# Performance work log

Measured on AMD Instinct MI355X. Metric: run time of the kernel, lower is better.

## Reference

```python
import jax, jax.numpy as jnp
import numpy as np

B, G, CE, D, L, H, DH, M, KQ = 4, 64, 384, 512, 8, 16, 32, 2048, 16
NJ, NB = 163, 11
DET_THRESH = 0.3
PATCH = 14.0
EPS = 1e-8


def _ln(x, g, b):
    mu = x.mean(-1, keepdims=True)
    v = x.var(-1, keepdims=True)
    return (x - mu) * jax.lax.rsqrt(v + 1e-5) * g + b


def setup_inputs():
    key = jax.random.key(0)
    ks = iter(jax.random.split(key, 64))
    def n(sh, s=0.02):
        return (jax.random.normal(next(ks), sh) * s).astype(jnp.float32)
    inp = {}
    inp['feat'] = jax.random.normal(next(ks), (B, G, G, CE), dtype=jnp.float32)
    inp['scores'] = jax.random.uniform(next(ks), (B, G, G), dtype=jnp.float32)
    inp['K_cam'] = jnp.tile(jnp.array([[1000., 0., 448.], [0., 1000., 448.], [0., 0., 1.]], dtype=jnp.float32), (B, 1, 1))
    inp['pos_emb'] = n((G * G, D), 1.0)
    inp['Wtok'] = n((CE, D)); inp['btok'] = jnp.zeros((D,), jnp.float32)
    for nm in ['Wq', 'Wk', 'Wv', 'Wo']:
        inp[nm] = n((L, D, D))
    inp['g1'] = jnp.ones((L, D), jnp.float32); inp['b1n'] = jnp.zeros((L, D), jnp.float32)
    inp['W1'] = n((L, D, M)); inp['bf1'] = jnp.zeros((L, M), jnp.float32)
    inp['W2'] = n((L, M, D)); inp['bf2'] = jnp.zeros((L, D), jnp.float32)
    inp['g2'] = jnp.ones((L, D), jnp.float32); inp['b2n'] = jnp.zeros((L, D), jnp.float32)
    inp['offW1'] = n((D, D)); inp['offb1'] = jnp.zeros((D,), jnp.float32)
    inp['offW2'] = n((D, 2)); inp['offb2'] = jnp.zeros((2,), jnp.float32)
    inp['dW1'] = n((D, D)); inp['db1'] = jnp.zeros((D,), jnp.float32)
    inp['dW2'] = n((D, 1)); inp['db2'] = jnp.zeros((1,), jnp.float32)
    inp['sW1'] = n((D, D)); inp['sb1'] = jnp.zeros((D,), jnp.float32)
    inp['sW2'] = n((D, NB)); inp['sb2'] = jnp.zeros((NB,), jnp.float32)
    inp['pW1'] = n((D + NJ * 6, D)); inp['pb1'] = jnp.zeros((D,), jnp.float32)
    inp['pW2'] = n((D, NJ * 6)); inp['pb2'] = jnp.zeros((NJ * 6,), jnp.float32)
    # identity-like 6D init pose per joint: eye(3)[:, :2].flatten() = [1,0,0,1,0,0]
    inp['init_body_pose'] = jnp.tile(jnp.array([1., 0., 0., 1., 0., 0.], dtype=jnp.float32), NJ)
    inp['useful_rotmat'] = (jax.random.uniform(next(ks), (NJ,)) < 0.66).astype(jnp.float32)
    return inp


def reference(feat, scores, K_cam, pos_emb, Wtok, btok,
              Wq, Wk, Wv, Wo, g1, b1n, W1, bf1, W2, bf2, g2, b2n,
              offW1, offb1, offW2, offb2, dW1, db1, dW2, db2,
              sW1, sb1, sW2, sb2, pW1, pb1, pW2, pb2,
              init_body_pose, useful_rotmat):
    # --- NMS via 3x3 max-pool (stride 1, same padding) + threshold ---
    sm = jax.lax.reduce_window(scores, -jnp.inf, jax.lax.max, (1, 3, 3), (1, 1, 1), 'SAME')
    sc = scores * (sm == scores).astype(scores.dtype)
    flat = sc.reshape(B, G * G)
    vals, idx = jax.lax.top_k(flat, KQ)                 # padded ragged detections
    mask = (vals >= DET_THRESH).astype(feat.dtype)      # [B,KQ] validity mask
    row = idx // G
    col = idx % G
    # --- token projection + 2d pos emb, gather queries ---
    dec_emb = feat @ Wtok + btok + pos_emb.reshape(G, G, D)        # [B,G,G,D]
    ctx = dec_emb.reshape(B, G * G, D)                              # context per image
    q = jnp.take_along_axis(ctx, idx[..., None], axis=1)            # [B,KQ,D]
    x = q * mask[..., None]
    scale = DH ** -0.5
    # --- HPH decoder: depth x (prenorm cross-attn to full-image context + FFN) ---
    for l in range(L):
        h = _ln(x, g1[l], b1n[l])
        qh = (h @ Wq[l]).reshape(B, KQ, H, DH)
        kh = (ctx @ Wk[l]).reshape(B, G * G, H, DH)
        vh = (ctx @ Wv[l]).reshape(B, G * G, H, DH)
        att = jax.nn.softmax(jnp.einsum('bqhd,bkhd->bhqk', qh, kh) * scale, axis=-1)
        o = jnp.einsum('bhqk,bkhd->bqhd', att, vh).reshape(B, KQ, H * DH) @ Wo[l]
        x = x + o * mask[..., None]
        h2 = _ln(x, g2[l], b2n[l])
        x = x + (jax.nn.gelu(h2 @ W1[l] + bf1[l]) @ W2[l] + bf2[l]) * mask[..., None]
    y = x.reshape(B * KQ, D)
    m = mask.reshape(B * KQ, 1)
    # --- heads ---
    offset = jax.nn.relu(y @ offW1 + offb1) @ offW2 + offb2          # [N,2]
    loc_coarse = jnp.stack([col.reshape(-1), row.reshape(-1)], -1).astype(y.dtype)
    loc = (loc_coarse + 0.5 + offset) * PATCH
    Kd = jnp.repeat(K_cam, KQ, axis=0)                               # [N,3,3]
    focal = Kd[:, 0, 0]
    d_raw = jax.nn.relu(y @ dW1 + db1) @ dW2 + db2                   # [N,1]
    dist = focal[:, None] / jnp.clip(jnp.exp(d_raw), 1e-5)
    homo = jnp.concatenate([loc, jnp.ones_like(loc[:, :1])], -1)     # [N,3]
    Kinv = jnp.linalg.inv(Kd)
    transl = jnp.einsum('nij,nj->ni', Kinv, homo) * dist             # [N,3]
    shape_ = jax.nn.sigmoid(jax.nn.relu(y @ sW1 + sb1) @ sW2 + sb2)  # [N,11]
    ibp = jnp.broadcast_to(init_body_pose, (B * KQ, NJ * 6))
    rot6d = jax.nn.relu(jnp.concatenate([y, ibp], -1) @ pW1 + pb1) @ pW2 + pb2 + ibp
    # --- special Gram-Schmidt: 6D -> rotation matrices ---
    Mm = rot6d.reshape(-1, NJ, 3, 2)
    u0 = Mm[..., 0]
    u0 = u0 / (jnp.linalg.norm(u0, axis=-1, keepdims=True) + EPS)
    v1 = Mm[..., 1] - jnp.sum(Mm[..., 1] * u0, -1, keepdims=True) * u0
    u1 = v1 / (jnp.linalg.norm(v1, axis=-1, keepdims=True) + EPS)
    u2 = jnp.cross(u0, u1)
    rotmat = jnp.stack([u0, u1, u2], -1)                             # [N,NJ,3,3]
    eye = jnp.eye(3, dtype=rotmat.dtype)
    um = useful_rotmat.reshape(1, NJ, 1, 1)
    rotmat = um * rotmat + (1.0 - um) * eye
    out = jnp.concatenate([loc, offset, dist, transl, shape_, rotmat.reshape(B * KQ, NJ * 9)], -1) * m
    return out
```

## Files before the change

### kernel.cpp

```cpp
#include <hip/hip_runtime.h>

typedef unsigned int uint;
typedef unsigned short u16;

#define BB 4
#define CE 384
#define DD 512
#define LL 8
#define HH 16
#define MM 2048
#define NJ 163
#define TOK 4096
#define BKQ 64
#define QH 256
#define OUTW 1486
#define NROT 978
#define QKSCALE 0.17677669529663687f

typedef __attribute__((ext_vector_type(8))) short short8;
typedef __attribute__((ext_vector_type(4))) float float4v;

static __device__ __forceinline__ u16 f2bf(float f){
  union { float f; uint u; } c; c.f = f;
  uint u = c.u;
// ... 6 lines not shown
static __device__ __forceinline__ float wred_sum(float v){
  for (int o = 32; o; o >>= 1) v += __shfl_xor(v, o, 64);
  return v;
}
static __device__ __forceinline__ void gl16(const void* g, void* l){
  __builtin_amdgcn_global_load_lds((const __attribute__((address_space(1))) void*)g,
                                   (__attribute__((address_space(3))) void*)l, 16, 0, 0);
}

__global__ __launch_bounds__(256) void k_nms_topk(const float* __restrict__ scores,
    int* __restrict__ oidx, float* __restrict__ omask, float* __restrict__ ocol, float* __restrict__ orow)
{
  int b = blockIdx.x, t = threadIdx.x;
  __shared__ float sraw[4096];
  __shared__ float sv[4]; __shared__ int si[4]; __shared__ int swin;
  const float* sp = scores + (size_t)b * 4096;
  for (int i = t; i < 4096; i += 256) sraw[i] = sp[i];
  __syncthreads();
  float v[16];
  #pragma unroll
  for (int j = 0; j < 16; j++){
    int i = t + j*256;
    int r = i >> 6, c = i & 63;
    float mx = -1e30f;
    for (int dr = -1; dr <= 1; dr++){
      int rr = r + dr; if (rr < 0 || rr > 63) continue;
      for (int dc = -1; dc <= 1; dc++){
        int cc = c + dc; if (cc < 0 || cc > 63) continue;
        mx = fmaxf(mx, sraw[rr*64+cc]);
      }
    }
    float s = sraw[i];
    v[j] = (s == mx) ? s : 0.0f;
  }
  int lane = t & 63, wv = t >> 6;
  for (int iter = 0; iter < 16; iter++){
    float best = -1e30f; int bi_ = 1 << 30;
    #pragma unroll
    for (int j = 0; j < 16; j++){
      if (v[j] > best){ best = v[j]; bi_ = t + j*256; }
    }
    #pragma unroll
    for (int o = 32; o; o >>= 1){
      float ov = __shfl_xor(best, o, 64);
      int oi = __shfl_xor(bi_, o, 64);
      if (ov > best || (ov == best && oi < bi_)){ best = ov; bi_ = oi; }
    }
    if (lane == 0){ sv[wv] = best; si[wv] = bi_; }
    __syncthreads();
    if (t == 0){
      float bb = sv[0]; int ii = si[0];
      for (int k = 1; k < 4; k++){
        if (sv[k] > bb || (sv[k] == bb && si[k] < ii)){ bb = sv[k]; ii = si[k]; }
      }
      oidx[b*16+iter] = ii;
      omask[b*16+iter] = (bb >= 0.3f) ? 1.f : 0.f;
      ocol[b*16+iter] = (float)(ii & 63);
      orow[b*16+iter] = (float)(ii >> 6);
      swin = ii;
    }
    __syncthreads();
    int wi = swin;
    if ((wi & 255) == t) v[wi >> 8] = -1e30f;
    __syncthreads();
  }
}

__global__ __launch_bounds__(256) void k_cvt_bf16(const float* __restrict__ in, u16* __restrict__ out, int n4){
  int i = blockIdx.x*256 + threadIdx.x;
  int stride = gridDim.x*256;
  for (int j = i; j < n4; j += stride){
    float4 v = ((const float4*)in)[j];
    ushort4 o;
    o.x = f2bf(v.x); o.y = f2bf(v.y); o.z = f2bf(v.z); o.w = f2bf(v.w);
    ((ushort4*)out)[j] = o;
  }
}

struct PJobs {
  const float* s[24]; u16* d[24];
  int R[24], C[24], t0[25];
  int njobs, ntiles;
};
__global__ __launch_bounds__(256) void k_prepw(PJobs J){
  __shared__ float tile[32][33];
  for (int g = blockIdx.x; g < J.ntiles; g += gridDim.x){
    int j = 0;
    while (g >= J.t0[j+1]) j++;
    int ti = g - J.t0[j];
    int C_ = J.C[j], R_ = J.R[j];
    int tC = (C_ + 31) >> 5;
    int ry = ti / tC, cx = ti - ry*tC;
    int c0 = cx*32, r0 = ry*32;
    int tx = threadIdx.x & 31, ty = threadIdx.x >> 5;
    const float* src = J.s[j]; u16* dst = J.d[j];
    for (int i = 0; i < 32; i += 8){
      float v = 0.f;
      if (c0+tx < C_) v = src[(size_t)(r0+ty+i)*C_ + c0+tx];
      tile[ty+i][tx] = v;
    }
    __syncthreads();
    for (int i = 0; i < 32; i += 8){
      if (c0+ty+i < C_) dst[(size_t)(c0+ty+i)*R_ + r0+tx] = f2bf(tile[tx][ty+i]);
    }
    __syncthreads();
  }
}

__global__ __launch_bounds__(256) void k_transp_b(const u16* __restrict__ in, u16* __restrict__ out, int R, int C){
  in  += (size_t)blockIdx.z * R * C;
  out += (size_t)blockIdx.z * R * C;
  __shared__ u16 tile[32][33];
  int c0 = blockIdx.x*32, r0 = blockIdx.y*32;
  int tx = threadIdx.x & 31, ty = threadIdx.x >> 5;
  for (int i = 0; i < 32; i += 8) tile[ty+i][tx] = in[(size_t)(r0+ty+i)*C + c0+tx];
  __syncthreads();
  for (int i = 0; i < 32; i += 8) out[(size_t)(c0+ty+i)*R + r0+tx] = tile[tx][ty+i];
}

__global__ __launch_bounds__(256) void k_wqk(const float* __restrict__ wq, const float* __restrict__ wk,
    u16* __restrict__ AT)
{
  __shared__ __align__(16) u16 As[2560];
  __shared__ __align__(16) u16 Bs[2560];
  int id = blockIdx.x, t = threadIdx.x;
  int rt = id & 127, dt = id >> 7;
  int h = rt >> 3, dout0 = (rt & 7)*64, din0 = dt*64;
  int r = t >> 2, c0 = (t & 3)*8;
  {
    float4 u0 = *(const float4*)(wk + (size_t)(dout0+r)*DD + h*32 + c0);
    float4 u1 = *(const float4*)(wk + (size_t)(dout0+r)*DD + h*32 + c0 + 4);
    u16* d = As + r*40 + c0;
    d[0]=f2bf(u0.x); d[1]=f2bf(u0.y); d[2]=f2bf(u0.z); d[3]=f2bf(u0.w);
    d[4]=f2bf(u1.x); d[5]=f2bf(u1.y); d[6]=f2bf(u1.z); d[7]=f2bf(u1.w);
    float4 v0 = *(const float4*)(wq + (size_t)(din0+r)*DD + h*32 + c0);
    float4 v1 = *(const float4*)(wq + (size_t)(din0+r)*DD + h*32 + c0 + 4);
    u16* e = Bs + r*40 + c0;
    e[0]=f2bf(v0.x); e[1]=f2bf(v0.y); e[2]=f2bf(v0.z); e[3]=f2bf(v0.w);
    e[4]=f2bf(v1.x); e[5]=f2bf(v1.y); e[6]=f2bf(v1.z); e[7]=f2bf(v1.w);
  }
  __syncthreads();
  int lane = t & 63, w = t >> 6, lr = lane & 15, lk = lane >> 4;
  short8 af = *(const short8*)&As[(w*16+lr)*40 + lk*8];
  float4v acc[4];
  float4v z4 = {0.f,0.f,0.f,0.f};
  acc[0]=z4; acc[1]=z4; acc[2]=z4; acc[3]=z4;
  #pragma unroll
  for (int nf = 0; nf < 4; nf++){
    short8 bf8 = *(const short8*)&Bs[(nf*16+lr)*40 + lk*8];
    acc[nf] = __builtin_amdgcn_mfma_f32_16x16x32_bf16(af, bf8, acc[nf], 0, 0, 0);
  }
  #pragma unroll
  for (int nf = 0; nf < 4; nf++){
    #pragma unroll
    for (int jj = 0; jj < 4; jj++){
      int row = w*16 + lk*4 + jj;
      AT[(size_t)(h*512 + dout0 + row)*DD + din0 + nf*16 + lr] = f2bf(acc[nf][jj]*QKSCALE);
    }
  }
}

__global__ __launch_bounds__(256) void k_wvo(const float* __restrict__ wv, const float* __restrict__ wo,
    u16* __restrict__ WVOT)
{
  __shared__ __align__(16) u16 As[2560];
  __shared__ __align__(16) u16 Bs[2560];
  int id = blockIdx.x, t = threadIdx.x;
  int ct = id & 127, dt = id >> 7;
  int h = ct >> 3, Dc0 = (ct & 7)*64, dout0 = dt*64;
  {
    int c = t >> 3, d8 = (t & 7)*8;
    float4 a0 = *(const float4*)(wo + (size_t)(h*32+c)*DD + dout0 + d8);
    float4 a1 = *(const float4*)(wo + (size_t)(h*32+c)*DD + dout0 + d8 + 4);
    As[(d8+0)*40 + c] = f2bf(a0.x);
    As[(d8+1)*40 + c] = f2bf(a0.y);
    As[(d8+2)*40 + c] = f2bf(a0.z);
    As[(d8+3)*40 + c] = f2bf(a0.w);
    As[(d8+4)*40 + c] = f2bf(a1.x);
    As[(d8+5)*40 + c] = f2bf(a1.y);
    As[(d8+6)*40 + c] = f2bf(a1.z);
    As[(d8+7)*40 + c] = f2bf(a1.w);
    int r = t >> 2, c0 = (t & 3)*8;
    float4 v0 = *(const float4*)(wv + (size_t)(Dc0+r)*DD + h*32 + c0);
    float4 v1 = *(const float4*)(wv + (size_t)(Dc0+r)*DD + h*32 + c0 + 4);
    u16* e = Bs + r*40 + c0;
    e[0]=f2bf(v0.x); e[1]=f2bf(v0.y); e[2]=f2bf(v0.z); e[3]=f2bf(v0.w);
    e[4]=f2bf(v1.x); e[5]=f2bf(v1.y); e[6]=f2bf(v1.z); e[7]=f2bf(v1.w);
  }
  __syncthreads();
  int lane = t & 63, w = t >> 6, lr = lane & 15, lk = lane >> 4;
  short8 af = *(const short8*)&As[(w*16+lr)*40 + lk*8];
  float4v acc[4];
  float4v z4 = {0.f,0.f,0.f,0.f};
  acc[0]=z4; acc[1]=z4; acc[2]=z4; acc[3]=z4;
  #pragma unroll
  for (int nf = 0; nf < 4; nf++){
    short8 bf8 = *(const short8*)&Bs[(nf*16+lr)*40 + lk*8];
    acc[nf] = __builtin_amdgcn_mfma_f32_16x16x32_bf16(af, bf8, acc[nf], 0, 0, 0);
  }
  #pragma unroll
  for (int nf = 0; nf < 4; nf++){
    #pragma unroll
    for (int jj = 0; jj < 4; jj++){
      int row = w*16 + lk*4 + jj;
      WVOT[(size_t)(dout0 + row)*8192 + h*512 + Dc0 + nf*16 + lr] = f2bf(acc[nf][jj]);
    }
  }
}

__global__ __launch_bounds__(256) void k_red8(const float* __restrict__ parts, u16* __restrict__ cf){
  int i4 = blockIdx.x*256 + threadIdx.x;
  int elem = i4*4;
  int row = elem >> 13, col = elem & 8191;
  int b = row >> 4, q = row & 15, h = col >> 9, Dc = col & 511;
  const float* src = parts + ((size_t)b*8)*131072 + (size_t)(q*16+h)*512 + Dc;
  float4 s = *(const float4*)src;
  #pragma unroll
  for (int ks = 1; ks < 8; ks++){
    float4 g = *(const float4*)(src + (size_t)ks*131072);
    s.x += g.x; s.y += g.y; s.z += g.z; s.w += g.w;
  }
  ushort4 o;
  o.x = f2bf(s.x); o.y = f2bf(s.y); o.z = f2bf(s.z); o.w = f2bf(s.w);
  *(ushort4*)&cf[(size_t)row*8192 + col] = o;
}

__global__ __launch_bounds__(256) void k_gemm_emb(
    const u16* __restrict__ A, const u16* __restrict__ Bt, u16* __restrict__ Cb,
    const float* __restrict__ ep1, const float* __restrict__ ep2)
{
  int m0 = blockIdx.y*128, n0 = blockIdx.x*128;
  __shared__ __align__(16) u16 As[128*64];
  __shared__ __align__(16) u16 Bs[128*64];
  int t = threadIdx.x, lane = t & 63, wave = t >> 6;
  int wr = wave >> 1, wc = wave & 1;
  int lr = lane & 15, lk = lane >> 4;
  int sr8 = t >> 3, sl = t & 7;
  int sw = ((sl ^ (sr8 & 7)) * 8);
  float4v acc[4][4];
  float4v z4 = {0.f, 0.f, 0.f, 0.f};
  #pragma unroll
  for (int i = 0; i < 4; i++)
    #pragma unroll
    for (int j = 0; j < 4; j++) acc[i][j] = z4;
  for (int kt = 0; kt < CE; kt += 64){
    __syncthreads();
    #pragma unroll
    for (int rg = 0; rg < 4; rg++){
      gl16(A + (size_t)(m0 + rg*32 + sr8)*CE + kt + sw, As + rg*2048 + 8*t);
      gl16(Bt + (size_t)(n0 + rg*32 + sr8)*CE + kt + sw, Bs + rg*2048 + 8*t);
    }
    __syncthreads();
    #pragma unroll
    for (int s = 0; s < 2; s++){
      int slot = ((s*4 + lk) ^ (lr & 7)) * 8;
      short8 af[4], bfr[4];
      #pragma unroll
      for (int i = 0; i < 4; i++) af[i] = *(const short8*)&As[(wr*64 + i*16 + lr)*64 + slot];
      #pragma unroll
      for (int j = 0; j < 4; j++) bfr[j] = *(const short8*)&Bs[(wc*64 + j*16 + lr)*64 + slot];
      #pragma unroll
      for (int i = 0; i < 4; i++)
        #pragma unroll
        for (int j = 0; j < 4; j++)
          acc[i][j] = __builtin_amdgcn_mfma_f32_16x16x32_bf16(af[i], bfr[j], acc[i][j], 0, 0, 0);
    }
  }
  #pragma unroll
  for (int i = 0; i < 4; i++){
    int rbase = m0 + wr*64 + i*16 + lk*4;
    #pragma unroll
    for (int j = 0; j < 4; j++){
      int cc = n0 + wc*64 + j*16 + lr;
      #pragma unroll
      for (int jj = 0; jj < 4; jj++){
        int rr = rbase + jj;
        float vv = acc[i][j][jj] + ep1[cc] + ep2[(size_t)(rr & 4095)*DD + cc];
        Cb[(size_t)rr*DD + cc] = f2bf(vv);
      }
    }
  }
}

__global__ __launch_bounds__(256) void k_misc(const float* __restrict__ feat, const float* __restrict__ Wtok,
    const float* __restrict__ btok, const float* __restrict__ pos_emb, const int* __restrict__ oidx,
    float* __restrict__ x, const float* __restrict__ pW1, const float* __restrict__ pb1,
    const float* __restrict__ ibp, float* __restrict__ hb4,
    const float* __restrict__ offb1, const float* __restrict__ db1, const float* __restrict__ sb1,
    const float* __restrict__ pb2, float* __restrict__ cvec2)
{
  int bid = blockIdx.x, t = threadIdx.x;
  if (bid < 64){
    int b = bid >> 4, tok = oidx[bid];
    __shared__ float fs[CE];
    const float* fr = feat + ((size_t)b*TOK + tok) * CE;
    for (int i = t; i < CE; i += 256) fs[i] = fr[i];
    __syncthreads();
    for (int d = t; d < DD; d += 256){
      float acc = btok[d] + pos_emb[(size_t)tok*DD + d];
      for (int i = 0; i < CE; i++) acc += fs[i] * Wtok[(size_t)i*DD + d];
      x[(size_t)bid*DD + d] = acc;
    }
  } else if (bid < 192){
    int d = (bid - 64)*4 + (t >> 6);
    int ln = t & 63;
    float acc = 0.f;
    for (int i = ln; i < NJ*6; i += 64) acc += ibp[i] * pW1[(size_t)(DD+i)*DD + d];
    acc = wred_sum(acc);
    if (ln == 0) hb4[1536 + d] = acc + pb1[d];
  } else {
    for (int i = t; i < 1536; i += 256)
      hb4[i] = (i < 512) ? offb1[i] : (i < 1024 ? db1[i-512] : sb1[i-1024]);
    for (int i = t; i < 1024; i += 256)
      cvec2[i] = (i < NJ*6) ? (pb2[i] + ibp[i]) : 0.f;
  }
}

template<int EPI>
__global__ __launch_bounds__(256) void k_gemm_bt64(
    const u16* __restrict__ A, const u16* __restrict__ Bt,
    float* __restrict__ C, u16* __restrict__ Cb,
    int Kslice, int lda, int ldb, int ldc,
    long sA, long sB, long sC, int ksplit)
{
  int bz = blockIdx.z;
  int batch = bz / ksplit, ks = bz - batch*ksplit;
  const u16* Ab = A + (size_t)batch*sA + (size_t)ks*Kslice;
  const u16* Bb = Bt + (size_t)batch*sB + (size_t)ks*Kslice;
  int m0 = blockIdx.y*128, n0 = blockIdx.x*64;
  __shared__ __align__(16) u16 As[128*64];
  __shared__ __align__(16) u16 Bs[64*64];
  int t = threadIdx.x, lane = t & 63, w = t >> 6;
  int lr = lane & 15, lk = lane >> 4;
  int sr8 = t >> 3, sl = t & 7;
  int sw = ((sl ^ (sr8 & 7)) * 8);
  float4v acc[2][4];
  float4v z4 = {0.f,0.f,0.f,0.f};
  #pragma unroll
  for (int i = 0; i < 2; i++)
    #pragma unroll
    for (int j = 0; j < 4; j++) acc[i][j] = z4;

  for (int kt = 0; kt < Kslice; kt += 64){
    __syncthreads();
    #pragma unroll
    for (int rg = 0; rg < 4; rg++)
      gl16(Ab + (size_t)(m0 + rg*32 + sr8)*lda + kt + sw, As + rg*2048 + 8*t);
    #pragma unroll
    for (int rg = 0; rg < 2; rg++)
      gl16(Bb + (size_t)(n0 + rg*32 + sr8)*ldb + kt + sw, Bs + rg*2048 + 8*t);
    __syncthreads();
    #pragma unroll
    for (int s = 0; s < 2; s++){
      int slot = ((s*4 + lk) ^ (lr & 7)) * 8;
      short8 af[2], bfr[4];
      #pragma unroll
      for (int i = 0; i < 2; i++) af[i] = *(const short8*)&As[(w*32 + i*16 + lr)*64 + slot];
      #pragma unroll
      for (int j = 0; j < 4; j++) bfr[j] = *(const short8*)&Bs[(j*16 + lr)*64 + slot];
      #pragma unroll
      for (int i = 0; i < 2; i++)
        #pragma unroll
        for (int j = 0; j < 4; j++)
          acc[i][j] = __builtin_amdgcn_mfma_f32_16x16x32_bf16(af[i], bfr[j], acc[i][j], 0, 0, 0);
    }
  }
  #pragma unroll
  for (int i = 0; i < 2; i++){
    int rbase = m0 + w*32 + i*16 + lk*4;
    #pragma unroll
    for (int j = 0; j < 4; j++){
      int cc = n0 + j*16 + lr;
      #pragma unroll
      for (int jj = 0; jj < 4; jj++){
        int rr = rbase + jj;
        if (EPI == 0) C[(size_t)bz*sC + (size_t)rr*ldc + cc] = acc[i][j][jj];
        else Cb[(size_t)batch*sC + (size_t)rr*ldc + cc] = f2bf(acc[i][j][jj]);
      }
    }
  }
}

template<int ACT, int RES, int OUTB, int DOLN, int NG, int HPB, int ZMAP = 0>
__global__ __launch_bounds__(256) void k_mf64(
    const u16* __restrict__ A, const float* __restrict__ xf,
    const float* __restrict__ g, const float* __restrict__ bb,
    const u16* __restrict__ Bt, const float* __restrict__ bias,
    float* __restrict__ C, u16* __restrict__ Cb, u16* __restrict__ Cb2,
    int N, int K, int kper, int ldc, float alpha)
{
  __shared__ __align__(16) u16 Asl[DOLN ? 64*520 : 64*64];
  __shared__ __align__(16) u16 Bs[64*64];
  int t = threadIdx.x, lane = t & 63, w = t >> 6;
  int lr = lane & 15, lk = lane >> 4;
  int n0 = blockIdx.x*64;
  int ks = blockIdx.y, kbeg = ks*kper;
  int sr8 = t >> 3, sl = t & 7;
  int sw = ((sl ^ (sr8 & 7)) * 8);

  if (DOLN){
    for (int rr = 0; rr < 16; rr++){
      int row = w*16 + rr;
      const float* xr = xf + (size_t)row*DD;
      float4 v0 = *(const float4*)(xr + lane*4);
      float4 v1 = *(const float4*)(xr + 256 + lane*4);
      float s = v0.x+v0.y+v0.z+v0.w + v1.x+v1.y+v1.z+v1.w;
      s = wred_sum(s);
      float mu = s * (1.f/DD);
      float d0=v0.x-mu, d1=v0.y-mu, d2=v0.z-mu, d3=v0.w-mu;
      float e0=v1.x-mu, e1=v1.y-mu, e2=v1.z-mu, e3=v1.w-mu;
      float q = d0*d0+d1*d1+d2*d2+d3*d3 + e0*e0+e1*e1+e2*e2+e3*e3;
      q = wred_sum(q);
      float inv = rsqrtf(q * (1.f/DD) + 1e-5f);
      float4 g0 = *(const float4*)(g + lane*4);
      float4 g1 = *(const float4*)(g + 256 + lane*4);
      float4 b0 = *(const float4*)(bb + lane*4);
      float4 b1 = *(const float4*)(bb + 256 + lane*4);
      u16* dst = &Asl[row*520];
      dst[lane*4+0] = f2bf(d0*inv*g0.x + b0.x);
      dst[lane*4+1] = f2bf(d1*inv*g0.y + b0.y);
      dst[lane*4+2] = f2bf(d2*inv*g0.z + b0.z);
      dst[lane*4+3] = f2bf(d3*inv*g0.w + b0.w);
      dst[256+lane*4+0] = f2bf(e0*inv*g1.x + b1.x);
      dst[256+lane*4+1] = f2bf(e1*inv*g1.y + b1.y);
      dst[256+lane*4+2] = f2bf(e2*inv*g1.z + b1.z);
      dst[256+lane*4+3] = f2bf(e3*inv*g1.w + b1.w);
    }
  }

  float4v acc[4];
  float4v z4 = {0.f,0.f,0.f,0.f};
  acc[0]=z4; acc[1]=z4; acc[2]=z4; acc[3]=z4;

  for (int kc = kbeg; kc < kbeg + kper; kc += 64){
    __syncthreads();
    if (!DOLN){
      gl16(A + (size_t)sr8*K + kc + sw,        (u16*)Asl + 8*t);
      gl16(A + (size_t)(32+sr8)*K + kc + sw,   (u16*)Asl + 2048 + 8*t);
    }
    gl16(Bt + (size_t)(n0+sr8)*K + kc + sw,      (u16*)Bs + 8*t);
    gl16(Bt + (size_t)(n0+32+sr8)*K + kc + sw,   (u16*)Bs + 2048 + 8*t);
    __syncthreads();
    #pragma unroll
    for (int s = 0; s < 2; s++){
      int slot = ((s*4 + lk) ^ (lr & 7)) * 8;
      short8 af;
      if (DOLN) af = *(const short8*)&Asl[(w*16+lr)*520 + kc + s*32 + lk*8];
      else      af = *(const short8*)&Asl[(w*16+lr)*64 + slot];
      #pragma unroll
      for (int nf = 0; nf < 4; nf++){
        short8 bf8 = *(const short8*)&Bs[(nf*16+lr)*64 + slot];
        acc[nf] = __builtin_amdgcn_mfma_f32_16x16x32_bf16(af, bf8, acc[nf], 0, 0, 0);
      }
    }
  }
  #pragma unroll
  for (int nf = 0; nf < 4; nf++){
    int col = n0 + nf*16 + lr;
    float bsv = (bias && ks == 0) ? bias[col] : 0.f;
    #pragma unroll
// ... 105 lines not shown
    o[0] = l0*m; o[1] = l1*m; o[2] = off0*m; o[3] = off1*m; o[4] = dist*m;
    o[5] = tx*m; o[6] = ty*m; o[7] = dist*m;
    #pragma unroll
    for (int j = 0; j < 11; j++){ float sp = sout[3+j] + sb2[j]; o[8+j] = m / (1.f + expf(-sp)); }
  }
  if (t < NJ){
    const float* rp = rot6d + (size_t)bq*NROT + t*6;
    float a0 = rp[0], b0 = rp[1], a1 = rp[2], b1 = rp[3], a2 = rp[4], b2 = rp[5];
    float n0 = sqrtf(a0*a0 + a1*a1 + a2*a2);
    float i0 = 1.f / (n0 + 1e-8f);
    float u00 = a0*i0, u01 = a1*i0, u02 = a2*i0;
    float dt = b0*u00 + b1*u01 + b2*u02;
    float v0 = b0 - dt*u00, v1 = b1 - dt*u01, v2 = b2 - dt*u02;
    float n1 = sqrtf(v0*v0 + v1*v1 + v2*v2);
    float i1 = 1.f / (n1 + 1e-8f);
    float u10 = v0*i1, u11 = v1*i1, u12 = v2*i1;
    float u20 = u01*u12 - u02*u11;
    float u21 = u02*u10 - u00*u12;
    float u22 = u00*u11 - u01*u10;
    float um = useful[t], om = 1.f - um;
    float R00 = um*u00 + om, R01 = um*u10,      R02 = um*u20;
    float R10 = um*u01,      R11 = um*u11 + om, R12 = um*u21;
    float R20 = um*u02,      R21 = um*u12,      R22 = um*u22 + om;
    float* o = out + (size_t)bq*OUTW + 19 + t*9;
    o[0] = R00*m; o[1] = R01*m; o[2] = R02*m;
    o[3] = R10*m; o[4] = R11*m; o[5] = R12*m;
    o[6] = R20*m; o[7] = R21*m; o[8] = R22*m;
  }
}

extern "C" void kernel_launch(void* const* d_in, const int* in_sizes, int n_in,
                              void* d_out, int out_size, void* d_ws, size_t ws_size,
                              hipStream_t stream)
{
  const float* feat   = (const float*)d_in[0];
  const float* scores = (const float*)d_in[1];
  const float* K_cam  = (const float*)d_in[2];
  const float* pos_emb= (const float*)d_in[3];
  const float* Wtok   = (const float*)d_in[4];
  const float* btok   = (const float*)d_in[5];
  const float* Wq     = (const float*)d_in[6];
  const float* Wk     = (const float*)d_in[7];
  const float* Wv     = (const float*)d_in[8];
  const float* Wo     = (const float*)d_in[9];
  const float* g1     = (const float*)d_in[10];
  const float* b1n    = (const float*)d_in[11];
  const float* W1     = (const float*)d_in[12];
  const float* bf1    = (const float*)d_in[13];
  const float* W2     = (const float*)d_in[14];
  const float* bf2    = (const float*)d_in[15];
  const float* g2     = (const float*)d_in[16];
  const float* b2n    = (const float*)d_in[17];
  const float* offW1  = (const float*)d_in[18];
  const float* offb1  = (const float*)d_in[19];
  const float* offW2  = (const float*)d_in[20];
  const float* offb2  = (const float*)d_in[21];
  const float* dW1    = (const float*)d_in[22];
  const float* db1    = (const float*)d_in[23];
  const float* dW2    = (const float*)d_in[24];
  const float* db2    = (const float*)d_in[25];
  const float* sW1    = (const float*)d_in[26];
  const float* sb1    = (const float*)d_in[27];
  const float* sW2    = (const float*)d_in[28];
  const float* sb2    = (const float*)d_in[29];
  const float* pW1    = (const float*)d_in[30];
  const float* pb1    = (const float*)d_in[31];
  const float* pW2    = (const float*)d_in[32];
  const float* pb2    = (const float*)d_in[33];
  const float* ibp    = (const float*)d_in[34];
  const float* useful = (const float*)d_in[35];
  float* out = (float*)d_out;

  char* wsp = (char*)d_ws;
  size_t off = 0;
  auto alloc = [&](size_t bytes)->char*{
    char* p = wsp + off;
    off += (bytes + 255) & ~((size_t)255);
    return p;
  };
  int*   t_idx  = (int*)  alloc(BKQ*4);
  float* t_mask = (float*)alloc(BKQ*4);
  float* t_col  = (float*)alloc(BKQ*4);
  float* t_row  = (float*)alloc(BKQ*4);
  u16*   feat_bf= (u16*)  alloc((size_t)BB*TOK*CE*2);
  u16*   wtokT  = (u16*)  alloc((size_t)DD*CE*2);
  u16*   ctx_bf = (u16*)  alloc((size_t)BB*TOK*DD*2);
  u16*   ctxT_bf= (u16*)  alloc((size_t)BB*TOK*DD*2);
  u16*   ATb    = (u16*)  alloc((size_t)8192*DD*2);
  u16*   WVOb   = (u16*)  alloc((size_t)DD*8192*2);
  u16*   w1T    = (u16*)  alloc((size_t)LL*DD*MM*2);
  u16*   w2T    = (u16*)  alloc((size_t)LL*MM*DD*2);
  u16*   headsT = (u16*)  alloc((size_t)4*DD*DD*2);
  u16*   pw2T   = (u16*)  alloc((size_t)1024*DD*2);
  float* x      = (float*)alloc((size_t)BKQ*DD*4);
  u16*   x_bf   = (u16*)  alloc((size_t)BKQ*DD*2);
  u16*   z_bf   = (u16*)  alloc((size_t)BKQ*HH*DD*2);
  u16*   logits = (u16*)  alloc((size_t)BB*QH*TOK*2);
  u16*   att_bf = (u16*)  alloc((size_t)BB*QH*TOK*2);
  float* parts  = (float*)alloc((size_t)BB*8*QH*DD*4);
  u16*   c_flat = (u16*)  alloc((size_t)BKQ*8192*2);
  u16*   mid_bf = (u16*)  alloc((size_t)BKQ*MM*2);
  float* h4     = (float*)alloc((size_t)BKQ*2048*4);
  u16*   hp_bf  = (u16*)  alloc((size_t)BKQ*DD*2);
  float* hb4    = (float*)alloc(2048*4);
  float* cvec2  = (float*)alloc(1024*4);
  float* rot6d  = (float*)alloc((size_t)BKQ*NROT*4);
  if (off > ws_size) return;

  PJobs J;
  int ntl = 0, nj = 0;
  auto addjob = [&](const float* s, u16* d, int R, int C){
    J.s[nj] = s; J.d[nj] = d; J.R[nj] = R; J.C[nj] = C; J.t0[nj] = ntl;
    ntl += ((R+31)/32) * ((C+31)/32);
    nj++;
  };
  addjob(Wtok, wtokT, CE, DD);
  for (int l = 0; l < LL; l++) addjob(W1 + (size_t)l*DD*MM, w1T + (size_t)l*MM*DD, DD, MM);
  for (int l = 0; l < LL; l++) addjob(W2 + (size_t)l*MM*DD, w2T + (size_t)l*DD*MM, MM, DD);
  addjob(offW1, headsT,            DD, DD);
  addjob(dW1,   headsT + DD*DD,    DD, DD);
  addjob(sW1,   headsT + 2*DD*DD,  DD, DD);
  addjob(pW1,   headsT + 3*DD*DD,  DD, DD);
  addjob(pW2,   pw2T, DD, NROT);
  J.t0[nj] = ntl; J.njobs = nj; J.ntiles = ntl;

  k_nms_topk<<<BB, 256, 0, stream>>>(scores, t_idx, t_mask, t_col, t_row);
  k_cvt_bf16<<<3072, 256, 0, stream>>>(feat, feat_bf, BB*TOK*CE/4);
  k_prepw<<<2048, 256, 0, stream>>>(J);
  k_gemm_emb<<<dim3(DD/128, (BB*TOK)/128, 1), 256, 0, stream>>>(feat_bf, wtokT, ctx_bf, btok, pos_emb);
  k_transp_b<<<dim3(DD/32, TOK/32, BB), 256, 0, stream>>>(ctx_bf, ctxT_bf, TOK, DD);
  k_misc<<<193, 256, 0, stream>>>(feat, Wtok, btok, pos_emb, t_idx, x, pW1, pb1, ibp, hb4,
                                  offb1, db1, sb1, pb2, cvec2);

  for (int l = 0; l < LL; l++){
    k_wqk<<<1024, 256, 0, stream>>>(Wq + (size_t)l*DD*DD, Wk + (size_t)l*DD*DD, ATb);
    k_mf64<0,0,0,1,0,0,1><<<dim3(128,1), 256, 0, stream>>>(
        nullptr, x, g1 + l*DD, b1n + l*DD, ATb, nullptr,
        nullptr, z_bf, nullptr, 8192, DD, DD, DD, 1.f);
    k_gemm_bt64<1><<<dim3(TOK/64, 2, BB), 256, 0, stream>>>(
        z_bf, ctx_bf, nullptr, logits,
        DD, DD, DD, TOK, (long)QH*DD, (long)TOK*DD, (long)QH*TOK, 1);
    k_softmax<<<BB*QH, 256, 0, stream>>>(logits, att_bf);
    k_gemm_bt64<0><<<dim3(DD/64, 2, BB*8), 256, 0, stream>>>(
        att_bf, ctxT_bf, parts, nullptr,
        TOK/8, TOK, TOK, DD, (long)QH*TOK, (long)DD*TOK, (long)QH*DD, 8);
    k_wvo<<<1024, 256, 0, stream>>>(Wv + (size_t)l*DD*DD, Wo + (size_t)l*DD*DD, WVOb);
    k_red8<<<512, 256, 0, stream>>>(parts, c_flat);
    k_mf64<0,1,0,0,0,0,0><<<dim3(8,16), 256, 0, stream>>>(
        c_flat, nullptr, nullptr, nullptr, WVOb, nullptr,
        x, nullptr, nullptr, DD, 8192, 512, DD, 1.f);
    k_mf64<2,0,1,1,0,0,0><<<dim3(MM/64,1), 256, 0, stream>>>(
        nullptr, x, g2 + l*DD, b2n + l*DD, w1T + (size_t)l*DD*MM, bf1 + l*MM,
        nullptr, mid_bf, nullptr, MM, DD, DD, MM, 1.f);
    k_mf64<0,1,0,0,0,0,0><<<dim3(8,8), 256, 0, stream>>>(
        mid_bf, nullptr, nullptr, nullptr, w2T + (size_t)l*MM*DD, bf2 + l*DD,
        x, nullptr, nullptr, DD, MM, MM/8, DD, 1.f);
  }

  k_cvt_bf16<<<32, 256, 0, stream>>>(x, x_bf, BKQ*DD/4);
  k_mf64<1,0,0,0,0,1,0><<<dim3(32,1), 256, 0, stream>>>(
      x_bf, nullptr, nullptr, nullptr, headsT, hb4,
      h4, nullptr, hp_bf, 2048, DD, DD, 2048, 1.f);
  k_mf64<0,0,0,0,1,0,0><<<dim3(16,1), 256, 0, stream>>>(
      hp_bf, nullptr, nullptr, nullptr, pw2T, cvec2,
      rot6d, nullptr, nullptr, NROT, DD, DD, NROT, 1.f);
  k_final<<<BKQ, 256, 0, stream>>>(h4, rot6d, offW2, offb2, dW2, db2, sW2, sb2,
                                   K_cam, useful, t_mask, t_col, t_row, out);
}
```

Before: 964.6 us.

## Fuse feat conversion and transpose into embed GEMM, merge weight prep kernels, bf16 split-K parts

Converts fp32 feat to bf16 inside the embedding GEMM load and writes the transposed context from shared memory in its epilogue, removing the separate conversion and transpose kernels. Merges the Wq·Wk and Wv·Wo precompute kernels into one launch and folds bias prep into the weight-prep kernel. Stores split-K attention partials in bf16 to halve their traffic, and gathers query tokens from the bf16 context instead of recomputing them in fp32. This trades some precision (bf16 partial sums and initial queries) for fewer launches and less memory traffic.

```diff
diff --git a/kernel.cpp b/kernel.cpp
--- a/kernel.cpp
+++ b/kernel.cpp
@@ -112,9 +112,28 @@
   int R[24], C[24], t0[25];
   int njobs, ntiles;
 };
-__global__ __launch_bounds__(256) void k_prepw(PJobs J){
+__global__ __launch_bounds__(256) void k_prep_all(PJobs J,
+    const float* __restrict__ pW1, const float* __restrict__ pb1,
+    const float* __restrict__ ibp, float* __restrict__ hb4,
+    const float* __restrict__ offb1, const float* __restrict__ db1, const float* __restrict__ sb1,
+    const float* __restrict__ pb2, float* __restrict__ cvec2)
+{
+  int bid = blockIdx.x, t = threadIdx.x;
+  if (bid < 128){
+    int d = bid*4 + (t >> 6);
+    int ln = t & 63;
+    float acc = 0.f;
+    for (int i = ln; i < NJ*6; i += 64) acc += ibp[i] * pW1[(size_t)(DD+i)*DD + d];
+    acc = wred_sum(acc);
+    if (ln == 0) hb4[1536 + d] = acc + pb1[d];
+  } else if (bid == 128){
+    for (int i = t; i < 1536; i += 256)
+      hb4[i] = (i < 512) ? offb1[i] : (i < 1024 ? db1[i-512] : sb1[i-1024]);
+    for (int i = t; i < 1024; i += 256)
+      cvec2[i] = (i < NJ*6) ? (pb2[i] + ibp[i]) : 0.f;
+  }
   __shared__ float tile[32][33];
-  for (int g = blockIdx.x; g < J.ntiles; g += gridDim.x){
+  for (int g = bid; g < J.ntiles; g += gridDim.x){
     int j = 0;
     while (g >= J.t0[j+1]) j++;
     int ti = g - J.t0[j];
@@ -122,7 +141,7 @@
     int tC = (C_ + 31) >> 5;
     int ry = ti / tC, cx = ti - ry*tC;
     int c0 = cx*32, r0 = ry*32;
-    int tx = threadIdx.x & 31, ty = threadIdx.x >> 5;
+    int tx = t & 31, ty = t >> 5;
     const float* src = J.s[j]; u16* dst = J.d[j];
     for (int i = 0; i < 32; i += 8){
       float v = 0.f;
@@ -137,131 +156,116 @@
   }
 }
 
-__global__ __launch_bounds__(256) void k_transp_b(const u16* __restrict__ in, u16* __restrict__ out, int R, int C){
-  in  += (size_t)blockIdx.z * R * C;
-  out += (size_t)blockIdx.z * R * C;
-  __shared__ u16 tile[32][33];
-  int c0 = blockIdx.x*32, r0 = blockIdx.y*32;
-  int tx = threadIdx.x & 31, ty = threadIdx.x >> 5;
-  for (int i = 0; i < 32; i += 8) tile[ty+i][tx] = in[(size_t)(r0+ty+i)*C + c0+tx];
-  __syncthreads();
-  for (int i = 0; i < 32; i += 8) out[(size_t)(c0+ty+i)*R + r0+tx] = tile[tx][ty+i];
-}
-
-__global__ __launch_bounds__(256) void k_wqk(const float* __restrict__ wq, const float* __restrict__ wk,
-    u16* __restrict__ AT)
+__global__ __launch_bounds__(256) void k_wqkvo(const float* __restrict__ wq, const float* __restrict__ wk,
+    const float* __restrict__ wv, const float* __restrict__ wo,
+    u16* __restrict__ AT, u16* __restrict__ WVOT)
 {
   __shared__ __align__(16) u16 As[2560];
   __shared__ __align__(16) u16 Bs[2560];
-  int id = blockIdx.x, t = threadIdx.x;
-  int rt = id & 127, dt = id >> 7;
-  int h = rt >> 3, dout0 = (rt & 7)*64, din0 = dt*64;
-  int r = t >> 2, c0 = (t & 3)*8;
-  {
-    float4 u0 = *(const float4*)(wk + (size_t)(dout0+r)*DD + h*32 + c0);
-    float4 u1 = *(const float4*)(wk + (size_t)(dout0+r)*DD + h*32 + c0 + 4);
-    u16* d = As + r*40 + c0;
-    d[0]=f2bf(u0.x); d[1]=f2bf(u0.y); d[2]=f2bf(u0.z); d[3]=f2bf(u0.w);
-    d[4]=f2bf(u1.x); d[5]=f2bf(u1.y); d[6]=f2bf(u1.z); d[7]=f2bf(u1.w);
-    float4 v0 = *(const float4*)(wq + (size_t)(din0+r)*DD + h*32 + c0);
-    float4 v1 = *(const float4*)(wq + (size_t)(din0+r)*DD + h*32 + c0 + 4);
-    u16* e = Bs + r*40 + c0;
-    e[0]=f2bf(v0.x); e[1]=f2bf(v0.y); e[2]=f2bf(v0.z); e[3]=f2bf(v0.w);
-    e[4]=f2bf(v1.x); e[5]=f2bf(v1.y); e[6]=f2bf(v1.z); e[7]=f2bf(v1.w);
-  }
-  __syncthreads();
+  int t = threadIdx.x;
   int lane = t & 63, w = t >> 6, lr = lane & 15, lk = lane >> 4;
-  short8 af = *(const short8*)&As[(w*16+lr)*40 + lk*8];
   float4v acc[4];
   float4v z4 = {0.f,0.f,0.f,0.f};
   acc[0]=z4; acc[1]=z4; acc[2]=z4; acc[3]=z4;
-  #pragma unroll
-  for (int nf = 0; nf < 4; nf++){
-    short8 bf8 = *(const short8*)&Bs[(nf*16+lr)*40 + lk*8];
-    acc[nf] = __builtin_amdgcn_mfma_f32_16x16x32_bf16(af, bf8, acc[nf], 0, 0, 0);
-  }
-  #pragma unroll
-  for (int nf = 0; nf < 4; nf++){
-    #pragma unroll
-    for (int jj = 0; jj < 4; jj++){
-      int row = w*16 + lk*4 + jj;
-      AT[(size_t)(h*512 + dout0 + row)*DD + din0 + nf*16 + lr] = f2bf(acc[nf][jj]*QKSCALE);
-    }
-  }
-}
-
-__global__ __launch_bounds__(256) void k_wvo(const float* __restrict__ wv, const float* __restrict__ wo,
-    u16* __restrict__ WVOT)
-{
-  __shared__ __align__(16) u16 As[2560];
-  __shared__ __align__(16) u16 Bs[2560];
-  int id = blockIdx.x, t = threadIdx.x;
-  int ct = id & 127, dt = id >> 7;
-  int h = ct >> 3, Dc0 = (ct & 7)*64, dout0 = dt*64;
-  {
-    int c = t >> 3, d8 = (t & 7)*8;
-    float4 a0 = *(const float4*)(wo + (size_t)(h*32+c)*DD + dout0 + d8);
-    float4 a1 = *(const float4*)(wo + (size_t)(h*32+c)*DD + dout0 + d8 + 4);
-    As[(d8+0)*40 + c] = f2bf(a0.x);
-    As[(d8+1)*40 + c] = f2bf(a0.y);
-    As[(d8+2)*40 + c] = f2bf(a0.z);
-    As[(d8+3)*40 + c] = f2bf(a0.w);
-    As[(d8+4)*40 + c] = f2bf(a1.x);
-    As[(d8+5)*40 + c] = f2bf(a1.y);
-    As[(d8+6)*40 + c] = f2bf(a1.z);
-    As[(d8+7)*40 + c] = f2bf(a1.w);
+  if (blockIdx.x < 1024){
+    int id = blockIdx.x;
+    int rt = id & 127, dt = id >> 7;
+    int h = rt >> 3, dout0 = (rt & 7)*64, din0 = dt*64;
     int r = t >> 2, c0 = (t & 3)*8;
-    float4 v0 = *(const float4*)(wv + (size_t)(Dc0+r)*DD + h*32 + c0);
-    float4 v1 = *(const float4*)(wv + (size_t)(Dc0+r)*DD + h*32 + c0 + 4);
-    u16* e = Bs + r*40 + c0;
-    e[0]=f2bf(v0.x); e[1]=f2bf(v0.y); e[2]=f2bf(v0.z); e[3]=f2bf(v0.w);
-    e[4]=f2bf(v1.x); e[5]=f2bf(v1.y); e[6]=f2bf(v1.z); e[7]=f2bf(v1.w);
-  }
-  __syncthreads();
-  int lane = t & 63, w = t >> 6, lr = lane & 15, lk = lane >> 4;
-  short8 af = *(const short8*)&As[(w*16+lr)*40 + lk*8];
-  float4v acc[4];
-  float4v z4 = {0.f,0.f,0.f,0.f};
-  acc[0]=z4; acc[1]=z4; acc[2]=z4; acc[3]=z4;
-  #pragma unroll
-  for (int nf = 0; nf < 4; nf++){
-    short8 bf8 = *(const short8*)&Bs[(nf*16+lr)*40 + lk*8];
-    acc[nf] = __builtin_amdgcn_mfma_f32_16x16x32_bf16(af, bf8, acc[nf], 0, 0, 0);
-  }
-  #pragma unroll
-  for (int nf = 0; nf < 4; nf++){
-    #pragma unroll
-    for (int jj = 0; jj < 4; jj++){
-      int row = w*16 + lk*4 + jj;
-      WVOT[(size_t)(dout0 + row)*8192 + h*512 + Dc0 + nf*16 + lr] = f2bf(acc[nf][jj]);
-    }
-  }
-}
-
-__global__ __launch_bounds__(256) void k_red8(const float* __restrict__ parts, u16* __restrict__ cf){
+    {
+      float4 u0 = *(const float4*)(wk + (size_t)(dout0+r)*DD + h*32 + c0);
+      float4 u1 = *(const float4*)(wk + (size_t)(dout0+r)*DD + h*32 + c0 + 4);
+      u16* d = As + r*40 + c0;
+      d[0]=f2bf(u0.x); d[1]=f2bf(u0.y); d[2]=f2bf(u0.z); d[3]=f2bf(u0.w);
+      d[4]=f2bf(u1.x); d[5]=f2bf(u1.y); d[6]=f2bf(u1.z); d[7]=f2bf(u1.w);
+      float4 v0 = *(const float4*)(wq + (size_t)(din0+r)*DD + h*32 + c0);
+      float4 v1 = *(const float4*)(wq + (size_t)(din0+r)*DD + h*32 + c0 + 4);
+      u16* e = Bs + r*40 + c0;
+      e[0]=f2bf(v0.x); e[1]=f2bf(v0.y); e[2]=f2bf(v0.z); e[3]=f2bf(v0.w);
+      e[4]=f2bf(v1.x); e[5]=f2bf(v1.y); e[6]=f2bf(v1.z); e[7]=f2bf(v1.w);
+    }
+    __syncthreads();
+    short8 af = *(const short8*)&As[(w*16+lr)*40 + lk*8];
+    #pragma unroll
+    for (int nf = 0; nf < 4; nf++){
+      short8 bf8 = *(const short8*)&Bs[(nf*16+lr)*40 + lk*8];
+      acc[nf] = __builtin_amdgcn_mfma_f32_16x16x32_bf16(af, bf8, acc[nf], 0, 0, 0);
+    }
+    #pragma unroll
+    for (int nf = 0; nf < 4; nf++){
+      #pragma unroll
+      for (int jj = 0; jj < 4; jj++){
+        int row = w*16 + lk*4 + jj;
+        AT[(size_t)(h*512 + dout0 + row)*DD + din0 + nf*16 + lr] = f2bf(acc[nf][jj]*QKSCALE);
+      }
+    }
+  } else {
+    int id = blockIdx.x - 1024;
+    int ct = id & 127, dt = id >> 7;
+    int h = ct >> 3, Dc0 = (ct & 7)*64, dout0 = dt*64;
+    {
+      int c = t >> 3, d8 = (t & 7)*8;
+      float4 a0 = *(const float4*)(wo + (size_t)(h*32+c)*DD + dout0 + d8);
+      float4 a1 = *(const float4*)(wo + (size_t)(h*32+c)*DD + dout0 + d8 + 4);
+      As[(d8+0)*40 + c] = f2bf(a0.x);
+      As[(d8+1)*40 + c] = f2bf(a0.y);
+      As[(d8+2)*40 + c] = f2bf(a0.z);
+      As[(d8+3)*40 + c] = f2bf(a0.w);
+      As[(d8+4)*40 + c] = f2bf(a1.x);
+      As[(d8+5)*40 + c] = f2bf(a1.y);
+      As[(d8+6)*40 + c] = f2bf(a1.z);
+      As[(d8+7)*40 + c] = f2bf(a1.w);
+      int r = t >> 2, c0 = (t & 3)*8;
+      float4 v0 = *(const float4*)(wv + (size_t)(Dc0+r)*DD + h*32 + c0);
+      float4 v1 = *(const float4*)(wv + (size_t)(Dc0+r)*DD + h*32 + c0 + 4);
+      u16* e = Bs + r*40 + c0;
+      e[0]=f2bf(v0.x); e[1]=f2bf(v0.y); e[2]=f2bf(v0.z); e[3]=f2bf(v0.w);
+      e[4]=f2bf(v1.x); e[5]=f2bf(v1.y); e[6]=f2bf(v1.z); e[7]=f2bf(v1.w);
+    }
+    __syncthreads();
+    short8 af = *(const short8*)&As[(w*16+lr)*40 + lk*8];
+    #pragma unroll
+    for (int nf = 0; nf < 4; nf++){
+      short8 bf8 = *(const short8*)&Bs[(nf*16+lr)*40 + lk*8];
+      acc[nf] = __builtin_amdgcn_mfma_f32_16x16x32_bf16(af, bf8, acc[nf], 0, 0, 0);
+    }
+    #pragma unroll
+    for (int nf = 0; nf < 4; nf++){
+      #pragma unroll
+      for (int jj = 0; jj < 4; jj++){
+        int row = w*16 + lk*4 + jj;
+        WVOT[(size_t)(dout0 + row)*8192 + h*512 + Dc0 + nf*16 + lr] = f2bf(acc[nf][jj]);
+      }
+    }
+  }
+}
+
+__global__ __launch_bounds__(256) void k_red8(const u16* __restrict__ parts, u16* __restrict__ cf){
   int i4 = blockIdx.x*256 + threadIdx.x;
   int elem = i4*4;
   int row = elem >> 13, col = elem & 8191;
   int b = row >> 4, q = row & 15, h = col >> 9, Dc = col & 511;
-  const float* src = parts + ((size_t)b*8)*131072 + (size_t)(q*16+h)*512 + Dc;
-  float4 s = *(const float4*)src;
-  #pragma unroll
-  for (int ks = 1; ks < 8; ks++){
-    float4 g = *(const float4*)(src + (size_t)ks*131072);
-    s.x += g.x; s.y += g.y; s.z += g.z; s.w += g.w;
+  const u16* src = parts + ((size_t)b*8)*131072 + (size_t)(q*16+h)*512 + Dc;
+  float s0 = 0.f, s1 = 0.f, s2 = 0.f, s3 = 0.f;
+  #pragma unroll
+  for (int ks = 0; ks < 8; ks++){
+    ushort4 g = *(const ushort4*)(src + (size_t)ks*131072);
+    s0 += bf2f(g.x); s1 += bf2f(g.y); s2 += bf2f(g.z); s3 += bf2f(g.w);
   }
   ushort4 o;
-  o.x = f2bf(s.x); o.y = f2bf(s.y); o.z = f2bf(s.z); o.w = f2bf(s.w);
+  o.x = f2bf(s0); o.y = f2bf(s1); o.z = f2bf(s2); o.w = f2bf(s3);
   *(ushort4*)&cf[(size_t)row*8192 + col] = o;
 }
 
 __global__ __launch_bounds__(256) void k_gemm_emb(
-    const u16* __restrict__ A, const u16* __restrict__ Bt, u16* __restrict__ Cb,
+    const float* __restrict__ feat, const u16* __restrict__ Bt,
+    u16* __restrict__ ctx, u16* __restrict__ ctxT,
     const float* __restrict__ ep1, const float* __restrict__ ep2)
 {
+  __shared__ __align__(16) u16 SM[16640];
+  u16* As = SM;
+  u16* Bs = SM + 8192;
   int m0 = blockIdx.y*128, n0 = blockIdx.x*128;
-  __shared__ __align__(16) u16 As[128*64];
-  __shared__ __align__(16) u16 Bs[128*64];
   int t = threadIdx.x, lane = t & 63, wave = t >> 6;
   int wr = wave >> 1, wc = wave & 1;
   int lr = lane & 15, lk = lane >> 4;
@@ -276,10 +280,16 @@
   for (int kt = 0; kt < CE; kt += 64){
     __syncthreads();
     #pragma unroll
-    for (int rg = 0; rg < 4; rg++){
-      gl16(A + (size_t)(m0 + rg*32 + sr8)*CE + kt + sw, As + rg*2048 + 8*t);
+    for (int p = 0; p < 8; p++){
+      int r = (t >> 4) + p*16, f4 = t & 15;
+      float4 v = *(const float4*)&feat[(size_t)(m0+r)*CE + kt + f4*4];
+      int dc = ((f4 >> 1) ^ (r & 7))*8 + (f4 & 1)*4;
+      ushort4 o; o.x = f2bf(v.x); o.y = f2bf(v.y); o.z = f2bf(v.z); o.w = f2bf(v.w);
+      *(ushort4*)&As[r*64 + dc] = o;
+    }
+    #pragma unroll
+    for (int rg = 0; rg < 4; rg++)
       gl16(Bt + (size_t)(n0 + rg*32 + sr8)*CE + kt + sw, Bs + rg*2048 + 8*t);
-    }
     __syncthreads();
     #pragma unroll
     for (int s = 0; s < 2; s++){
@@ -296,6 +306,7 @@
           acc[i][j] = __builtin_amdgcn_mfma_f32_16x16x32_bf16(af[i], bfr[j], acc[i][j], 0, 0, 0);
     }
   }
+  __syncthreads();
   #pragma unroll
   for (int i = 0; i < 4; i++){
     int rbase = m0 + wr*64 + i*16 + lk*4;
@@ -306,44 +317,31 @@
       for (int jj = 0; jj < 4; jj++){
         int rr = rbase + jj;
         float vv = acc[i][j][jj] + ep1[cc] + ep2[(size_t)(rr & 4095)*DD + cc];
-        Cb[(size_t)rr*DD + cc] = f2bf(vv);
+        u16 bv = f2bf(vv);
+        ctx[(size_t)rr*DD + cc] = bv;
+        SM[(cc - n0)*130 + (rr - m0)] = bv;
       }
     }
   }
-}
-
-__global__ __launch_bounds__(256) void k_misc(const float* __restrict__ feat, const float* __restrict__ Wtok,
-    const float* __restrict__ btok, const float* __restrict__ pos_emb, const int* __restrict__ oidx,
-    float* __restrict__ x, const float* __restrict__ pW1, const float* __restrict__ pb1,
-    const float* __restrict__ ibp, float* __restrict__ hb4,
-    const float* __restrict__ offb1, const float* __restrict__ db1, const float* __restrict__ sb1,
-    const float* __restrict__ pb2, float* __restrict__ cvec2)
-{
-  int bid = blockIdx.x, t = threadIdx.x;
-  if (bid < 64){
-    int b = bid >> 4, tok = oidx[bid];
-    __shared__ float fs[CE];
-    const float* fr = feat + ((size_t)b*TOK + tok) * CE;
-    for (int i = t; i < CE; i += 256) fs[i] = fr[i];
-    __syncthreads();
-    for (int d = t; d < DD; d += 256){
-      float acc = btok[d] + pos_emb[(size_t)tok*DD + d];
-      for (int i = 0; i < CE; i++) acc += fs[i] * Wtok[(size_t)i*DD + d];
-      x[(size_t)bid*DD + d] = acc;
-    }
-  } else if (bid < 192){
-    int d = (bid - 64)*4 + (t >> 6);
-    int ln = t & 63;
-    float acc = 0.f;
-    for (int i = ln; i < NJ*6; i += 64) acc += ibp[i] * pW1[(size_t)(DD+i)*DD + d];
-    acc = wred_sum(acc);
-    if (ln == 0) hb4[1536 + d] = acc + pb1[d];
-  } else {
-    for (int i = t; i < 1536; i += 256)
-      hb4[i] = (i < 512) ? offb1[i] : (i < 1024 ? db1[i-512] : sb1[i-1024]);
-    for (int i = t; i < 1024; i += 256)
-      cvec2[i] = (i < NJ*6) ? (pb2[i] + ibp[i]) : 0.f;
-  }
+  __syncthreads();
+  int b = m0 >> 12, tok0 = m0 & 4095;
+  int tx = t & 63, ty = t >> 6;
+  #pragma unroll 4
+  for (int it = 0; it < 32; it++){
+    int c = ty*32 + it;
+    uint vv = *(const uint*)&SM[c*130 + tx*2];
+    *(uint*)&ctxT[((size_t)b*DD + n0 + c)*TOK + tok0 + tx*2] = vv;
+  }
+}
+
+__global__ __launch_bounds__(256) void k_gather2(const u16* __restrict__ ctx, const int* __restrict__ oidx,
+    float* __restrict__ x)
+{
+  int bq = blockIdx.x, t = threadIdx.x;
+  int b = bq >> 4, tok = oidx[bq];
+  uint v = ((const uint*)(ctx + ((size_t)b*TOK + tok)*DD))[t];
+  float2 o; o.x = bf2f((u16)(v & 0xFFFF)); o.y = bf2f((u16)(v >> 16));
+  *(float2*)&x[(size_t)bq*DD + t*2] = o;
 }
 
 template<int EPI>
@@ -405,7 +403,8 @@
       for (int jj = 0; jj < 4; jj++){
         int rr = rbase + jj;
         if (EPI == 0) C[(size_t)bz*sC + (size_t)rr*ldc + cc] = acc[i][j][jj];
-        else Cb[(size_t)batch*sC + (size_t)rr*ldc + cc] = f2bf(acc[i][j][jj]);
+        else if (EPI == 1) Cb[(size_t)batch*sC + (size_t)rr*ldc + cc] = f2bf(acc[i][j][jj]);
+        else Cb[(size_t)bz*sC + (size_t)rr*ldc + cc] = f2bf(acc[i][j][jj]);
       }
     }
   }
@@ -677,7 +676,6 @@
   float* t_mask = (float*)alloc(BKQ*4);
   float* t_col  = (float*)alloc(BKQ*4);
   float* t_row  = (float*)alloc(BKQ*4);
-  u16*   feat_bf= (u16*)  alloc((size_t)BB*TOK*CE*2);
   u16*   wtokT  = (u16*)  alloc((size_t)DD*CE*2);
   u16*   ctx_bf = (u16*)  alloc((size_t)BB*TOK*DD*2);
   u16*   ctxT_bf= (u16*)  alloc((size_t)BB*TOK*DD*2);
@@ -692,7 +690,7 @@
   u16*   z_bf   = (u16*)  alloc((size_t)BKQ*HH*DD*2);
   u16*   logits = (u16*)  alloc((size_t)BB*QH*TOK*2);
   u16*   att_bf = (u16*)  alloc((size_t)BB*QH*TOK*2);
-  float* parts  = (float*)alloc((size_t)BB*8*QH*DD*4);
+  u16*   parts  = (u16*)  alloc((size_t)BB*8*QH*DD*2);
   u16*   c_flat = (u16*)  alloc((size_t)BKQ*8192*2);
   u16*   mid_bf = (u16*)  alloc((size_t)BKQ*MM*2);
   float* h4     = (float*)alloc((size_t)BKQ*2048*4);
@@ -720,15 +718,13 @@
   J.t0[nj] = ntl; J.njobs = nj; J.ntiles = ntl;
 
   k_nms_topk<<<BB, 256, 0, stream>>>(scores, t_idx, t_mask, t_col, t_row);
-  k_cvt_bf16<<<3072, 256, 0, stream>>>(feat, feat_bf, BB*TOK*CE/4);
-  k_prepw<<<2048, 256, 0, stream>>>(J);
-  k_gemm_emb<<<dim3(DD/128, (BB*TOK)/128, 1), 256, 0, stream>>>(feat_bf, wtokT, ctx_bf, btok, pos_emb);
-  k_transp_b<<<dim3(DD/32, TOK/32, BB), 256, 0, stream>>>(ctx_bf, ctxT_bf, TOK, DD);
-  k_misc<<<193, 256, 0, stream>>>(feat, Wtok, btok, pos_emb, t_idx, x, pW1, pb1, ibp, hb4,
-                                  offb1, db1, sb1, pb2, cvec2);
+  k_prep_all<<<2048, 256, 0, stream>>>(J, pW1, pb1, ibp, hb4, offb1, db1, sb1, pb2, cvec2);
+  k_gemm_emb<<<dim3(DD/128, (BB*TOK)/128, 1), 256, 0, stream>>>(feat, wtokT, ctx_bf, ctxT_bf, btok, pos_emb);
+  k_gather2<<<BKQ, 256, 0, stream>>>(ctx_bf, t_idx, x);
 
   for (int l = 0; l < LL; l++){
-    k_wqk<<<1024, 256, 0, stream>>>(Wq + (size_t)l*DD*DD, Wk + (size_t)l*DD*DD, ATb);
+    k_wqkvo<<<2048, 256, 0, stream>>>(Wq + (size_t)l*DD*DD, Wk + (size_t)l*DD*DD,
+                                      Wv + (size_t)l*DD*DD, Wo + (size_t)l*DD*DD, ATb, WVOb);
     k_mf64<0,0,0,1,0,0,1><<<dim3(128,1), 256, 0, stream>>>(
         nullptr, x, g1 + l*DD, b1n + l*DD, ATb, nullptr,
         nullptr, z_bf, nullptr, 8192, DD, DD, DD, 1.f);
@@ -736,10 +732,9 @@
         z_bf, ctx_bf, nullptr, logits,
         DD, DD, DD, TOK, (long)QH*DD, (long)TOK*DD, (long)QH*TOK, 1);
     k_softmax<<<BB*QH, 256, 0, stream>>>(logits, att_bf);
-    k_gemm_bt64<0><<<dim3(DD/64, 2, BB*8), 256, 0, stream>>>(
-        att_bf, ctxT_bf, parts, nullptr,
+    k_gemm_bt64<2><<<dim3(DD/64, 2, BB*8), 256, 0, stream>>>(
+        att_bf, ctxT_bf, nullptr, parts,
         TOK/8, TOK, TOK, DD, (long)QH*TOK, (long)DD*TOK, (long)QH*DD, 8);
-    k_wvo<<<1024, 256, 0, stream>>>(Wv + (size_t)l*DD*DD, Wo + (size_t)l*DD*DD, WVOb);
     k_red8<<<512, 256, 0, stream>>>(parts, c_flat);
     k_mf64<0,1,0,0,0,0,0><<<dim3(8,16), 256, 0, stream>>>(
         c_flat, nullptr, nullptr, nullptr, WVOb, nullptr,
```

After: 911.4 us. -5.5%, faster.
